# Performance work log

Measured on AMD Instinct MI355X. Metric: run time of the kernel, lower is better.

## Reference

```python
import jax, jax.numpy as jnp
import numpy as np

EPS = 1e-8
V_LAMBDA = 1.0
T_LAMBDA = 1.0
BB, DIM = 8192, 256


def _rowwise_cos(a, b):
    # torch.cosine_similarity semantics: dot / (max(|a|,eps) * max(|b|,eps))
    na = jnp.maximum(jnp.linalg.norm(a, axis=-1), EPS)
    nb = jnp.maximum(jnp.linalg.norm(b, axis=-1), EPS)
    return jnp.sum(a * b, axis=-1) / (na * nb)


def _clamped_normalize(x):
    n = jnp.maximum(jnp.linalg.norm(x, axis=-1, keepdims=True), EPS)
    return x / n


def _retrieval_acc(sim, labels):
    # sim: [v, t]; top-1 retrieval accuracy in percent
    return jnp.mean((jnp.argmax(sim, axis=-1) == labels).astype(jnp.float32)) * 100.0


def setup_inputs() -> dict:
    key = jax.random.key(0)
    ks = jax.random.split(key, 5)
    names = ['vis_pred', 'text_pred', 'vis_feats_proj', 'caption_emb', 'vis_feats_proj_narr']
    return {n: jax.random.normal(k, (BB, DIM), dtype=jnp.float32) for n, k in zip(names, ks)}


def reference(vis_pred, text_pred, vis_feats_proj, caption_emb, vis_feats_proj_narr):
    bb = vis_pred.shape[0]
    labels = jnp.arange(bb)

    # training losses (row-wise cosine similarity)
    vis_loss = jnp.mean(1.0 - _rowwise_cos(vis_pred, vis_feats_proj))
    text_loss = jnp.mean(1.0 - _rowwise_cos(text_pred, caption_emb))
    loss = V_LAMBDA * vis_loss + T_LAMBDA * text_loss

    # retrieval accuracies (no_grad block). The torch repeat_interleave/repeat +
    # elementwise cosine construction is exactly the pairwise cosine-sim matrix:
    # normalize rows once, then a [bb, dim] x [dim, bb] GEMM.
    v = _clamped_normalize(jax.lax.stop_gradient(vis_pred))
    gt_v = _clamped_normalize(jax.lax.stop_gradient(vis_feats_proj))
    narr_v = _clamped_normalize(jax.lax.stop_gradient(vis_feats_proj_narr))
    gt_t = _clamped_normalize(jax.lax.stop_gradient(caption_emb))
    # NOTE: in the original code both t_r and gt_t_r are tiles of gt_text, so
    # the 'text' side of every sim matrix is gt_t. We reproduce that faithfully.

    acc_gtv_gtt = _retrieval_acc(jnp.einsum('vd,td->vt', gt_v, gt_t), labels)
    acc_v_gtt = _retrieval_acc(jnp.einsum('vd,td->vt', v, gt_t), labels)
    acc_gtv_t = _retrieval_acc(jnp.einsum('vd,td->vt', gt_v, gt_t), labels)
    acc_v_t = _retrieval_acc(jnp.einsum('vd,td->vt', v, gt_t), labels)
    acc_narr_gtt = _retrieval_acc(jnp.einsum('vd,td->vt', narr_v, gt_t), labels)
    acc_narr_t = _retrieval_acc(jnp.einsum('vd,td->vt', narr_v, gt_t), labels)

    # order: vis_loss, text_loss, loss, gt_v-gt_t, v-gt_t, gt_v-t, v-t, narr_v-gt_t, narr_v-t
    return jnp.stack([vis_loss, text_loss, loss,
                      acc_gtv_gtt, acc_v_gtt, acc_gtv_t, acc_v_t,
                      acc_narr_gtt, acc_narr_t])
```

## Files before the change

kernel.cpp:

```cpp
#include <hip/hip_runtime.h>
#include <hip/hip_bf16.h>
#include <stdint.h>
#include <limits.h>

#define BB 8192
#define DIM 256

typedef __attribute__((ext_vector_type(4))) int int32x4;

__device__ __forceinline__ void load_lds16(const char* g, char* l) {
  __builtin_amdgcn_global_load_lds(
      (const __attribute__((address_space(1))) unsigned int*)g,
      (__attribute__((address_space(3))) unsigned int*)l, 16, 0, 0);
}

__device__ __forceinline__ float q8f(float x) {
  return rintf(fmaxf(fminf(x * 256.f, 127.f), -127.f));
}

__device__ __forceinline__ int imax(int a, int b) { return a > b ? a : b; }

__device__ __forceinline__ int dpp_max16(int u) {
  int t;
  t = __builtin_amdgcn_update_dpp(0, u, 0xB1, 0xF, 0xF, true);
  u = t > u ? t : u;
  t = __builtin_amdgcn_update_dpp(0, u, 0x4E, 0xF, 0xF, true);
  u = t > u ? t : u;
  t = __builtin_amdgcn_update_dpp(0, u, 0x124, 0xF, 0xF, true);
  u = t > u ? t : u;
  t = __builtin_amdgcn_update_dpp(0, u, 0x128, 0xF, 0xF, true);
  u = t > u ? t : u;
  return u;
}

__global__ __launch_bounds__(256) void phase1(
    const float* __restrict__ vp,  const float* __restrict__ tp,
    const float* __restrict__ vfp, const float* __restrict__ ce,
    const float* __restrict__ nr,
    float* __restrict__ rowcos, int* __restrict__ diag,
    char* __restrict__ abuf,
    char* __restrict__ gtbuf,
    int* __restrict__ maxComb, float* __restrict__ sums,
    int* __restrict__ ticket) {
  __shared__ unsigned ldsT[3][4][64];
  const int wave = threadIdx.x >> 6;
  const int lane = threadIdx.x & 63;
  const int row  = blockIdx.x * 4 + wave;
  const int base = row * DIM + lane * 4;

  float4 a = *(const float4*)&vp[base];
  float4 t = *(const float4*)&tp[base];
  float4 g = *(const float4*)&vfp[base];
  float4 c = *(const float4*)&ce[base];
  float4 n = *(const float4*)&nr[base];

  float s[7];
  s[0] = a.x*a.x + a.y*a.y + a.z*a.z + a.w*a.w;
  s[1] = g.x*g.x + g.y*g.y + g.z*g.z + g.w*g.w;
  s[2] = a.x*g.x + a.y*g.y + a.z*g.z + a.w*g.w;
  s[3] = t.x*t.x + t.y*t.y + t.z*t.z + t.w*t.w;
  s[4] = c.x*c.x + c.y*c.y + c.z*c.z + c.w*c.w;
  s[5] = t.x*c.x + t.y*c.y + t.z*c.z + t.w*c.w;
  s[6] = n.x*n.x + n.y*n.y + n.z*n.z + n.w*n.w;

  #pragma unroll
  for (int mk = 1; mk < 64; mk <<= 1) {
    #pragma unroll
    for (int q = 0; q < 7; ++q) s[q] += __shfl_xor(s[q], mk);
  }

  const float eps = 1e-8f;
  float na = fmaxf(sqrtf(s[0]), eps);
  float ng = fmaxf(sqrtf(s[1]), eps);
  float nt = fmaxf(sqrtf(s[3]), eps);
  float nc = fmaxf(sqrtf(s[4]), eps);
  float nn = fmaxf(sqrtf(s[6]), eps);
  float ia = 1.f / na, ig = 1.f / ng, ic = 1.f / nc, in_ = 1.f / nn;

  float qa0=q8f(a.x*ia), qa1=q8f(a.y*ia), qa2=q8f(a.z*ia), qa3=q8f(a.w*ia);
  float qg0=q8f(g.x*ig), qg1=q8f(g.y*ig), qg2=q8f(g.z*ig), qg3=q8f(g.w*ig);
  float qn0=q8f(n.x*in_),qn1=q8f(n.y*in_),qn2=q8f(n.z*in_),qn3=q8f(n.w*in_);
  float qc0=q8f(c.x*ic), qc1=q8f(c.y*ic), qc2=q8f(c.z*ic), qc3=q8f(c.w*ic);

  float d[3];
  d[0] = qg0*qc0 + qg1*qc1 + qg2*qc2 + qg3*qc3;
  d[1] = qa0*qc0 + qa1*qc1 + qa2*qc2 + qa3*qc3;
  d[2] = qn0*qc0 + qn1*qc1 + qn2*qc2 + qn3*qc3;
  #pragma unroll
  for (int mk = 1; mk < 64; mk <<= 1) {
    #pragma unroll
    for (int q = 0; q < 3; ++q) d[q] += __shfl_xor(d[q], mk);
  }

  auto pack = [](float x0, float x1, float x2, float x3) -> unsigned {
    return ((unsigned)((int)x0 & 0xFF)) | ((unsigned)((int)x1 & 0xFF) << 8) |
           ((unsigned)((int)x2 & 0xFF) << 16) | ((unsigned)((int)x3 & 0xFF) << 24);
  };
  ((unsigned*)gtbuf)[row * 64 + lane] = pack(qc0, qc1, qc2, qc3);
  ldsT[0][wave][lane] = pack(qg0, qg1, qg2, qg3);
  ldsT[1][wave][lane] = pack(qa0, qa1, qa2, qa3);
  ldsT[2][wave][lane] = pack(qn0, qn1, qn2, qn3);

  if (lane == 0) {
    rowcos[row]        = s[2] / (na * ng);
    rowcos[BB + row]   = s[5] / (nt * nc);
    diag[0 * BB + row] = (int)d[0];
    diag[1 * BB + row] = (int)d[1];
    diag[2 * BB + row] = (int)d[2];
    maxComb[0 * BB + row] = INT_MIN;
    maxComb[1 * BB + row] = INT_MIN;
    maxComb[2 * BB + row] = INT_MIN;
  }
  if (blockIdx.x == 0 && threadIdx.x < 5) sums[threadIdx.x] = 0.f;
  if (blockIdx.x == 0 && threadIdx.x == 5) *ticket = 0;

  __syncthreads();
  if (threadIdx.x < 192) {
    int mat = threadIdx.x >> 6, l = threadIdx.x & 63;
    int kc = l >> 2, j = l & 3;
    uint4 val = *(const uint4*)&ldsT[mat][j][kc * 4];
    int tileR = blockIdx.x >> 2;
    int rm    = (blockIdx.x & 3) * 4 + j;
    *(uint4*)&abuf[(size_t)mat * BB * DIM + tileR * 4096 + kc * 256 + rm * 16] = val;
  }
}

__global__ __launch_bounds__(256, 4) void sim_argmax(
    const char* __restrict__ Af, const char* __restrict__ B,
    int* __restrict__ maxComb) {
  __shared__ char Bs[128 * 256];
  __shared__ int comb[128][2];

  const int tid  = threadIdx.x;
  const int lane = tid & 63;
  const int wave = tid >> 6;
  const int wr   = wave >> 1, wc = wave & 1;
  const int m    = lane & 15, quad = lane >> 4;
  const int z    = blockIdx.z;

  const int rowTile = blockIdx.y * 128;
  const int colTile = blockIdx.x * 128;
  const char* Az = Af + (size_t)z * BB * DIM + (size_t)(rowTile >> 4) * 4096;
  const char* Bp = B + (size_t)colTile * DIM;

  #pragma unroll
  for (int t = 0; t < 8; ++t) {
    const int c   = t * 256 + tid;
    const int row = c >> 4;
    const int l   = (c & 15) ^ (row & 15);
    load_lds16(&Bp[row * DIM + l * 16], &Bs[c * 16]);
  }

  int32x4 acc[4][4];
  #pragma unroll
  for (int i = 0; i < 4; ++i)
    #pragma unroll
    for (int j = 0; j < 4; ++j) acc[i][j] = (int32x4){0, 0, 0, 0};

  int32x4 af[4];
  #pragma unroll
  for (int rt = 0; rt < 4; ++rt)
    af[rt] = *(const int32x4*)&Az[(size_t)(wr * 4 + rt) * 4096 + lane * 16];

  __syncthreads();

  #pragma unroll
  for (int kp = 0; kp < 4; ++kp) {
    int32x4 a[4];
    #pragma unroll
    for (int rt = 0; rt < 4; ++rt) a[rt] = af[rt];
    if (kp < 3) {
      #pragma unroll
      for (int rt = 0; rt < 4; ++rt)
        af[rt] = *(const int32x4*)&Az[(size_t)(wr * 4 + rt) * 4096 +
                                      (kp + 1) * 1024 + lane * 16];
    }
    int32x4 bf[4];
    #pragma unroll
    for (int ct = 0; ct < 4; ++ct) {
      int br = wc * 64 + ct * 16 + m;
      int p  = (kp * 4 + quad) ^ m;
      bf[ct] = *(const int32x4*)&Bs[br * 256 + p * 16];
    }
    #pragma unroll
    for (int rt = 0; rt < 4; ++rt)
      #pragma unroll
      for (int ct = 0; ct < 4; ++ct)
        acc[rt][ct] = __builtin_amdgcn_mfma_i32_16x16x64_i8(
            a[rt], bf[ct], acc[rt][ct], 0, 0, 0);
  }

  const int rowBase = rowTile + wr * 64;
  const int colBase = colTile + wc * 64;
  if (blockIdx.x != blockIdx.y) {
    const int addOne = (blockIdx.y > blockIdx.x) ? 1 : 0;
    #pragma unroll
    for (int rt = 0; rt < 4; ++rt) {
      #pragma unroll
      for (int reg = 0; reg < 4; ++reg) {
        int u = imax(imax(acc[rt][0][reg], acc[rt][1][reg]),
                     imax(acc[rt][2][reg], acc[rt][3][reg]));
        u = dpp_max16(u);
        if (m == 0)
          comb[wr * 64 + rt * 16 + quad * 4 + reg][wc] = u * 2 + addOne;
      }
    }
  } else {
    #pragma unroll
    for (int rt = 0; rt < 4; ++rt) {
      #pragma unroll
      for (int reg = 0; reg < 4; ++reg) {
        int i = rowBase + rt * 16 + quad * 4 + reg;
        int u = INT_MIN;
        #pragma unroll
        for (int ct = 0; ct < 4; ++ct) {
          int j = colBase + ct * 16 + m;
          int w = acc[rt][ct][reg] * 2 + ((j < i) ? 1 : 0);
          w = (j == i) ? INT_MIN : w;
          u = imax(u, w);
        }
        u = dpp_max16(u);
        if (m == 0) comb[wr * 64 + rt * 16 + quad * 4 + reg][wc] = u;
      }
    }
  }
  __syncthreads();
  if (tid < 128) {
    int u0 = comb[tid][0], u1 = comb[tid][1];
    atomicMax(&maxComb[(size_t)z * BB + rowTile + tid], imax(u0, u1));
  }
}

__global__ __launch_bounds__(256) void phase3_fin(
    const int* __restrict__ diag, const int* __restrict__ maxComb,
    const float* __restrict__ rowcos,
    float* __restrict__ sums, int* __restrict__ ticket,
    float* __restrict__ out) {
  __shared__ float red[4][5];
  __shared__ bool amLast;
  int r = blockIdx.x * 256 + threadIdx.x;
  int lane = threadIdx.x & 63, wave = threadIdx.x >> 6;
  float v[5];
  v[0] = rowcos[r];
  v[1] = rowcos[BB + r];
  #pragma unroll
  for (int z = 0; z < 3; ++z)
    v[2 + z] = (2 * diag[z * BB + r] >= maxComb[z * BB + r]) ? 1.f : 0.f;
  #pragma unroll
  for (int mk = 1; mk < 64; mk <<= 1) {
    #pragma unroll
    for (int q = 0; q < 5; ++q) v[q] += __shfl_xor(v[q], mk);
  }
  if (lane == 0) {
    #pragma unroll
    for (int q = 0; q < 5; ++q) red[wave][q] = v[q];
  }
  __syncthreads();
  if (threadIdx.x < 5) {
    float acc = red[0][threadIdx.x] + red[1][threadIdx.x] +
                red[2][threadIdx.x] + red[3][threadIdx.x];
    atomicAdd(&sums[threadIdx.x], acc);
  }
  __threadfence();
  __syncthreads();
  if (threadIdx.x == 0)
    amLast = (atomicAdd(ticket, 1) == (int)gridDim.x - 1);
  __syncthreads();
  if (amLast && threadIdx.x == 0) {
    float s0 = atomicAdd(&sums[0], 0.f);
    float s1 = atomicAdd(&sums[1], 0.f);
    float s2 = atomicAdd(&sums[2], 0.f);
    float s3 = atomicAdd(&sums[3], 0.f);
    float s4 = atomicAdd(&sums[4], 0.f);
    float vl = 1.f - s0 * (1.f / BB);
    float tl = 1.f - s1 * (1.f / BB);
    out[0] = vl;
    out[1] = tl;
    out[2] = vl + tl;
    float a0 = s2 * (100.f / BB);
    float a1 = s3 * (100.f / BB);
    float a2 = s4 * (100.f / BB);
    out[3] = a0;
    out[4] = a1;
    out[5] = a0;
    out[6] = a1;
    out[7] = a2;
    out[8] = a2;
  }
}

extern "C" void kernel_launch(void* const* d_in, const int* in_sizes, int n_in,
                              void* d_out, int out_size, void* d_ws, size_t ws_size,
                              hipStream_t stream) {
  const float* vp  = (const float*)d_in[0];
  const float* tp  = (const float*)d_in[1];
  const float* vfp = (const float*)d_in[2];
  const float* ce  = (const float*)d_in[3];
  const float* nr  = (const float*)d_in[4];

  char* ws = (char*)d_ws;
  float* sums    = (float*)ws;
  int*   ticket  = (int*)(ws + 32);
  int*   maxComb = (int*)(ws + 64);
  int*   diag    = maxComb + 3 * BB;
  float* rowcos  = (float*)(diag + 3 * BB);
  char*  abuf    = (char*)(rowcos + 2 * BB);
  char*  gtbuf   = abuf + (size_t)3 * BB * DIM;


  phase1<<<BB / 4, 256, 0, stream>>>(vp, tp, vfp, ce, nr, rowcos, diag,
                                     abuf, gtbuf, maxComb, sums, ticket);

  dim3 grid(BB / 128, BB / 128, 3);
  sim_argmax<<<grid, 256, 0, stream>>>(abuf, gtbuf, maxComb);

  phase3_fin<<<BB / 256, 256, 0, stream>>>(diag, maxComb, rowcos, sums, ticket,
                                           (float*)d_out);
}
```

Baseline: 150.3 us.

## Reuse staged B tile across all three A matrices in one block

The sim_argmax kernel no longer launches one block per A matrix along grid z. Each block now loads its 128-column B tile into LDS once and loops over the three A matrices, prefetching the next matrix's A fragments across the z boundary. This cuts the B global-to-LDS traffic and the block count to a third, and also saves per-block setup. In exchange each block does three times the work, and the grid shrinks to 4096 blocks, which may reduce latency hiding.

```diff
diff --git a/kernel.cpp b/kernel.cpp
--- a/kernel.cpp
+++ b/kernel.cpp
@@ -129,18 +129,17 @@
     const char* __restrict__ Af, const char* __restrict__ B,
     int* __restrict__ maxComb) {
   __shared__ char Bs[128 * 256];
-  __shared__ int comb[128][2];
+  __shared__ int comb[3][128][2];
 
   const int tid  = threadIdx.x;
   const int lane = tid & 63;
   const int wave = tid >> 6;
   const int wr   = wave >> 1, wc = wave & 1;
   const int m    = lane & 15, quad = lane >> 4;
-  const int z    = blockIdx.z;
 
   const int rowTile = blockIdx.y * 128;
   const int colTile = blockIdx.x * 128;
-  const char* Az = Af + (size_t)z * BB * DIM + (size_t)(rowTile >> 4) * 4096;
+  const char* A0 = Af + (size_t)(rowTile >> 4) * 4096;
   const char* Bp = B + (size_t)colTile * DIM;
 
   #pragma unroll
@@ -151,83 +150,95 @@
     load_lds16(&Bp[row * DIM + l * 16], &Bs[c * 16]);
   }
 
-  int32x4 acc[4][4];
-  #pragma unroll
-  for (int i = 0; i < 4; ++i)
-    #pragma unroll
-    for (int j = 0; j < 4; ++j) acc[i][j] = (int32x4){0, 0, 0, 0};
-
   int32x4 af[4];
   #pragma unroll
   for (int rt = 0; rt < 4; ++rt)
-    af[rt] = *(const int32x4*)&Az[(size_t)(wr * 4 + rt) * 4096 + lane * 16];
-
-  __syncthreads();
-
-  #pragma unroll
-  for (int kp = 0; kp < 4; ++kp) {
-    int32x4 a[4];
-    #pragma unroll
-    for (int rt = 0; rt < 4; ++rt) a[rt] = af[rt];
-    if (kp < 3) {
-      #pragma unroll
-      for (int rt = 0; rt < 4; ++rt)
-        af[rt] = *(const int32x4*)&Az[(size_t)(wr * 4 + rt) * 4096 +
-                                      (kp + 1) * 1024 + lane * 16];
-    }
-    int32x4 bf[4];
-    #pragma unroll
-    for (int ct = 0; ct < 4; ++ct) {
-      int br = wc * 64 + ct * 16 + m;
-      int p  = (kp * 4 + quad) ^ m;
-      bf[ct] = *(const int32x4*)&Bs[br * 256 + p * 16];
-    }
-    #pragma unroll
-    for (int rt = 0; rt < 4; ++rt)
-      #pragma unroll
-      for (int ct = 0; ct < 4; ++ct)
-        acc[rt][ct] = __builtin_amdgcn_mfma_i32_16x16x64_i8(
-            a[rt], bf[ct], acc[rt][ct], 0, 0, 0);
-  }
-
+    af[rt] = *(const int32x4*)&A0[(size_t)(wr * 4 + rt) * 4096 + lane * 16];
+
+  __syncthreads();
+
+  const bool offDiag = (blockIdx.x != blockIdx.y);
+  const int  addOne  = (blockIdx.y > blockIdx.x) ? 1 : 0;
   const int rowBase = rowTile + wr * 64;
   const int colBase = colTile + wc * 64;
-  if (blockIdx.x != blockIdx.y) {
-    const int addOne = (blockIdx.y > blockIdx.x) ? 1 : 0;
-    #pragma unroll
-    for (int rt = 0; rt < 4; ++rt) {
-      #pragma unroll
-      for (int reg = 0; reg < 4; ++reg) {
-        int u = imax(imax(acc[rt][0][reg], acc[rt][1][reg]),
-                     imax(acc[rt][2][reg], acc[rt][3][reg]));
-        u = dpp_max16(u);
-        if (m == 0)
-          comb[wr * 64 + rt * 16 + quad * 4 + reg][wc] = u * 2 + addOne;
+
+  #pragma unroll
+  for (int z = 0; z < 3; ++z) {
+    int32x4 acc[4][4];
+    #pragma unroll
+    for (int i = 0; i < 4; ++i)
+      #pragma unroll
+      for (int j = 0; j < 4; ++j) acc[i][j] = (int32x4){0, 0, 0, 0};
+
+    #pragma unroll
+    for (int kp = 0; kp < 4; ++kp) {
+      int32x4 a[4];
+      #pragma unroll
+      for (int rt = 0; rt < 4; ++rt) a[rt] = af[rt];
+      int nz = z, nkp = kp + 1;
+      if (nkp == 4) { nz = z + 1; nkp = 0; }
+      if (nz < 3) {
+        const char* An = A0 + (size_t)nz * BB * DIM;
+        #pragma unroll
+        for (int rt = 0; rt < 4; ++rt)
+          af[rt] = *(const int32x4*)&An[(size_t)(wr * 4 + rt) * 4096 +
+                                        nkp * 1024 + lane * 16];
+      }
+      int32x4 bf[4];
+      #pragma unroll
+      for (int ct = 0; ct < 4; ++ct) {
+        int br = wc * 64 + ct * 16 + m;
+        int p  = (kp * 4 + quad) ^ m;
+        bf[ct] = *(const int32x4*)&Bs[br * 256 + p * 16];
+      }
+      #pragma unroll
+      for (int rt = 0; rt < 4; ++rt)
+        #pragma unroll
+        for (int ct = 0; ct < 4; ++ct)
+          acc[rt][ct] = __builtin_amdgcn_mfma_i32_16x16x64_i8(
+              a[rt], bf[ct], acc[rt][ct], 0, 0, 0);
+    }
+
+    if (offDiag) {
+      #pragma unroll
+      for (int rt = 0; rt < 4; ++rt) {
+        #pragma unroll
+        for (int reg = 0; reg < 4; ++reg) {
+          int u = imax(imax(acc[rt][0][reg], acc[rt][1][reg]),
+                       imax(acc[rt][2][reg], acc[rt][3][reg]));
+          u = dpp_max16(u);
+          if (m == 0)
+            comb[z][wr * 64 + rt * 16 + quad * 4 + reg][wc] = u * 2 + addOne;
+        }
+      }
+    } else {
+      #pragma unroll
+      for (int rt = 0; rt < 4; ++rt) {
+        #pragma unroll
+        for (int reg = 0; reg < 4; ++reg) {
+          int i = rowBase + rt * 16 + quad * 4 + reg;
+          int u = INT_MIN;
+          #pragma unroll
+          for (int ct = 0; ct < 4; ++ct) {
+            int j = colBase + ct * 16 + m;
+            int w = acc[rt][ct][reg] * 2 + ((j < i) ? 1 : 0);
+            w = (j == i) ? INT_MIN : w;
+            u = imax(u, w);
+          }
+          u = dpp_max16(u);
+          if (m == 0) comb[z][wr * 64 + rt * 16 + quad * 4 + reg][wc] = u;
+        }
       }
     }
-  } else {
-    #pragma unroll
-    for (int rt = 0; rt < 4; ++rt) {
-      #pragma unroll
-      for (int reg = 0; reg < 4; ++reg) {
-        int i = rowBase + rt * 16 + quad * 4 + reg;
-        int u = INT_MIN;
-        #pragma unroll
-        for (int ct = 0; ct < 4; ++ct) {
-          int j = colBase + ct * 16 + m;
-          int w = acc[rt][ct][reg] * 2 + ((j < i) ? 1 : 0);
-          w = (j == i) ? INT_MIN : w;
-          u = imax(u, w);
-        }
-        u = dpp_max16(u);
-        if (m == 0) comb[wr * 64 + rt * 16 + quad * 4 + reg][wc] = u;
-      }
+  }
+
+  __syncthreads();
+  if (tid < 128) {
+    #pragma unroll
+    for (int z = 0; z < 3; ++z) {
+      int u = imax(comb[z][tid][0], comb[z][tid][1]);
+      atomicMax(&maxComb[(size_t)z * BB + rowTile + tid], u);
     }
-  }
-  __syncthreads();
-  if (tid < 128) {
-    int u0 = comb[tid][0], u1 = comb[tid][1];
-    atomicMax(&maxComb[(size_t)z * BB + rowTile + tid], imax(u0, u1));
   }
 }
 
@@ -311,7 +322,7 @@
   phase1<<<BB / 4, 256, 0, stream>>>(vp, tp, vfp, ce, nr, rowcos, diag,
                                      abuf, gtbuf, maxComb, sums, ticket);
 
-  dim3 grid(BB / 128, BB / 128, 3);
+  dim3 grid(BB / 128, BB / 128);
   sim_argmax<<<grid, 256, 0, stream>>>(abuf, gtbuf, maxComb);
 
   phase3_fin<<<BB / 256, 256, 0, stream>>>(diag, maxComb, rowcos, sums, ticket,
```

Result: slower. 236.6 us (+57.5%).
